# Performance work log

Measured on AMD Instinct MI355X. Metric: run time of the kernel, lower is better.

## Reference

```python
import jax, jax.numpy as jnp
import numpy as np
import math

INPUT_SZ = 1024
HIDDEN_SZ = 1024
BATCH = 64
SEQ = 512


def setup_inputs() -> dict:
    key = jax.random.key(0)
    ks = jax.random.split(key, 9)
    stdv = 1.0 / math.sqrt(HIDDEN_SZ)
    def u(k, shape):
        return jax.random.uniform(k, shape, jnp.float32, -stdv, stdv)
    W_shape = (INPUT_SZ + HIDDEN_SZ, HIDDEN_SZ)
    return {
        "x": jax.random.normal(ks[0], (BATCH, SEQ, INPUT_SZ), jnp.float32),
        "Wf": u(ks[1], W_shape), "bf": u(ks[2], (HIDDEN_SZ,)),
        "Wi": u(ks[3], W_shape), "bi": u(ks[4], (HIDDEN_SZ,)),
        "Wc": u(ks[5], W_shape), "bc": u(ks[6], (HIDDEN_SZ,)),
        "Wo": u(ks[7], W_shape), "bo": u(ks[8], (HIDDEN_SZ,)),
    }


def _lstm_cummax(x, Wf, bf, Wi, bi, Wc, bc, Wo, bo):
    B, S, _ = x.shape
    H = Wf.shape[1]
    # Concatenate the 4 gate matmuls into one GEMM (same math as 4 separate ones).
    W = jnp.concatenate([Wf, Wi, Wc, Wo], axis=1)  # (H+I, 4H)
    b = jnp.concatenate([bf, bi, bc, bo])          # (4H,)

    h0 = jnp.zeros((B, H), x.dtype)
    C0 = jnp.zeros((B, H), x.dtype)
    hmax0 = jnp.full((B, H), -jnp.inf, x.dtype)

    def step(carry, xt):
        h_in, Ct, hmax = carry
        hx = jnp.concatenate([h_in, xt], axis=1)   # (B, H+I), h first (matches torch cat((ht, xt)))
        g = hx @ W + b                             # (B, 4H)
        ft = jax.nn.sigmoid(g[:, :H])
        it = jax.nn.sigmoid(g[:, H:2 * H])
        cc = jnp.tanh(g[:, 2 * H:3 * H])
        ot = jax.nn.sigmoid(g[:, 3 * H:])
        Ct = ft * Ct + it * cc
        h = ot * jnp.tanh(Ct)                      # raw per-step hidden, stored in output seq
        hmax = jnp.maximum(hmax, h)                # running max over all steps so far
        # next-step input hidden is the running max (at t=0, max == h0 anyway)
        return (hmax, Ct, hmax), h

    (h_fin, C_fin, _), hs = jax.lax.scan(step, (h0, C0, hmax0), jnp.swapaxes(x, 0, 1))
    hidden_seq = jnp.swapaxes(hs, 0, 1)            # (B, S, H), raw per-step hiddens
    return hidden_seq, (h_fin, C_fin)


def reference(x, Wf, bf, Wi, bi, Wc, bc, Wo, bo):
    return _lstm_cummax(x, Wf, bf, Wi, bi, Wc, bc, Wo, bo)
```

## Files before the change

kernel.cpp:

```cpp
#include <hip/hip_runtime.h>
#include <hip/hip_bf16.h>
#include <math.h>
#include <stddef.h>

#define S_LEN 512
#define NBATCH 64
#define HID 1024
#define IN_SZ 1024
#define KTOT 2048
#define NB 128
#define NCOLS 32
#define JPB 8

using short8  = __attribute__((ext_vector_type(8))) short;
using floatx4 = __attribute__((ext_vector_type(4))) float;

static const size_t WPACK_OFF = 0;
static const size_t XBF_OFF   = 16777216;
static const size_t HBUF_OFF  = XBF_OFF + 67108864;
static const size_t FLAGS_OFF = HBUF_OFF + 67239936;

__device__ __forceinline__ unsigned short f2b(float f) {
  __hip_bfloat16 h = __float2bfloat16(f);
  return *reinterpret_cast<unsigned short*>(&h);
}
__device__ __forceinline__ float sigm(float z) {
  z = fminf(fmaxf(z, -30.f), 30.f);
  return 1.f / (1.f + __expf(-z));
}
__device__ __forceinline__ float tanh_(float z) {
  z = fminf(fmaxf(z, -15.f), 15.f);
  float e = __expf(2.f * z);
  return (e - 1.f) / (e + 1.f);
}

__global__ void prep_w(const float* __restrict__ Wf, const float* __restrict__ Wi,
                       const float* __restrict__ Wc, const float* __restrict__ Wo,
                       __hip_bfloat16* __restrict__ wpack) {
  __shared__ float tile[64][65];
  const int g = blockIdx.z;
  const float* W = (g == 0) ? Wf : (g == 1) ? Wi : (g == 2) ? Wc : Wo;
  const int k0 = blockIdx.x * 64, j0 = blockIdx.y * 64;
  const int tx = threadIdx.x, ty = threadIdx.y;
  for (int kk = 0; kk < 64; kk += 4)
    tile[kk + ty][tx] = W[(size_t)(k0 + kk + ty) * HID + j0 + tx];
  __syncthreads();
  for (int jj = 0; jj < 64; jj += 4) {
    int j = j0 + jj + ty;
    size_t out = ((size_t)((j >> 3) * NCOLS + g * 8 + (j & 7))) * KTOT + k0 + tx;
    wpack[out] = __float2bfloat16(tile[tx][jj + ty]);
  }
}

__global__ void prep_x(const float* __restrict__ x, unsigned short* __restrict__ xbf,
                       int* __restrict__ flags) {
  size_t i = ((size_t)blockIdx.x * blockDim.x + threadIdx.x) * 4;
  float4 v = *(const float4*)(x + i);
  ushort4 u;
  u.x = f2b(v.x); u.y = f2b(v.y); u.z = f2b(v.z); u.w = f2b(v.w);
  *(ushort4*)(xbf + i) = u;
  if (blockIdx.x == 0 && threadIdx.x < NB) flags[threadIdx.x] = 0;
}

__launch_bounds__(256, 1)
__global__ void lstm_rec(const unsigned short* __restrict__ xbf,
                         const unsigned short* __restrict__ wpack,
                         const float* __restrict__ bfv, const float* __restrict__ biv,
                         const float* __restrict__ bcv, const float* __restrict__ bov,
                         unsigned short* __restrict__ hbuf,
                         int* __restrict__ flags,
                         float* __restrict__ out) {
  __shared__ float part[4][64][36];
  const int tid  = threadIdx.x;
  const int w    = tid >> 6;
  const int lane = tid & 63;
  const int l15  = lane & 15;
  const int lq   = lane >> 4;
  const int p    = blockIdx.x;
  const int j0   = p * JPB;

  short8 Wreg[32];
  {
    const unsigned short* wp = wpack + (size_t)p * NCOLS * KTOT;
#pragma unroll
    for (int ks = 0; ks < 16; ++ks)
#pragma unroll
      for (int n = 0; n < 2; ++n) {
        int c = n * 16 + l15;
        int k = w * 512 + ks * 32 + lq * 8;
        Wreg[ks * 2 + n] = *(const short8*)(wp + (size_t)c * KTOT + k);
      }
  }
  float bias0, bias1;
  {
    int c = l15;
    bias0 = (c < 8) ? bfv[j0 + c] : biv[j0 + c - 8];
    bias1 = (c < 8) ? bcv[j0 + c] : bov[j0 + c - 8];
  }
  float Cst[4]  = {0.f, 0.f, 0.f, 0.f};
  float hmax[4] = {-__builtin_inff(), -__builtin_inff(), -__builtin_inff(), -__builtin_inff()};
  const int  jj    = l15 & 7;
  const bool act   = (l15 < 8);
  const int  bbase = w * 16 + lq * 4;
  const bool is_x  = (w >= 2);

  for (int t = 0; t < S_LEN; ++t) {
    floatx4 acc[4][2];
#pragma unroll
    for (int m = 0; m < 4; ++m) { acc[m][0] = (floatx4){0,0,0,0}; acc[m][1] = (floatx4){0,0,0,0}; }

    if (is_x) {
      const unsigned short* xa = xbf + (size_t)t * IN_SZ + (w - 2) * 512 + lq * 8;
      short8 a[16][4];
#pragma unroll
      for (int ks = 0; ks < 16; ++ks)
#pragma unroll
        for (int m = 0; m < 4; ++m)
          a[ks][m] = *(const short8*)(xa + (size_t)(m * 16 + l15) * ((size_t)S_LEN * IN_SZ) + ks * 32);
#pragma unroll
      for (int ks = 0; ks < 16; ++ks)
#pragma unroll
        for (int m = 0; m < 4; ++m) {
          acc[m][0] = __builtin_amdgcn_mfma_f32_16x16x32_bf16(a[ks][m], Wreg[ks * 2 + 0], acc[m][0], 0, 0, 0);
          acc[m][1] = __builtin_amdgcn_mfma_f32_16x16x32_bf16(a[ks][m], Wreg[ks * 2 + 1], acc[m][1], 0, 0, 0);
        }
    } else if (t > 0) {
      {
        bool ready;
        do {
          int a = __hip_atomic_load(&flags[lane],      __ATOMIC_RELAXED, __HIP_MEMORY_SCOPE_AGENT);
          int b = __hip_atomic_load(&flags[lane + 64], __ATOMIC_RELAXED, __HIP_MEMORY_SCOPE_AGENT);
          ready = __all((a >= t) && (b >= t));
        } while (!ready);
        __atomic_signal_fence(__ATOMIC_ACQUIRE);
      }
      const unsigned short* ha = hbuf + (size_t)t * (NBATCH * HID) + w * 512 + lq * 8;
      short8 a[16][4];
#pragma unroll
      for (int ks = 0; ks < 16; ++ks)
#pragma unroll
        for (int m = 0; m < 4; ++m)
          a[ks][m] = *(const short8*)(ha + (size_t)(m * 16 + l15) * HID + ks * 32);
#pragma unroll
      for (int ks = 0; ks < 16; ++ks)
#pragma unroll
        for (int m = 0; m < 4; ++m) {
          acc[m][0] = __builtin_amdgcn_mfma_f32_16x16x32_bf16(a[ks][m], Wreg[ks * 2 + 0], acc[m][0], 0, 0, 0);
          acc[m][1] = __builtin_amdgcn_mfma_f32_16x16x32_bf16(a[ks][m], Wreg[ks * 2 + 1], acc[m][1], 0, 0, 0);
        }
    }
#pragma unroll
    for (int m = 0; m < 4; ++m) {
      *(floatx4*)&part[w][lane][m * 8 + 0] = acc[m][0];
      *(floatx4*)&part[w][lane][m * 8 + 4] = acc[m][1];
    }
    __syncthreads();
    floatx4 r0 = {0, 0, 0, 0}, r1 = {0, 0, 0, 0};
#pragma unroll
    for (int sw = 0; sw < 4; ++sw) {
      r0 += *(const floatx4*)&part[sw][lane][w * 8 + 0];
      r1 += *(const floatx4*)&part[sw][lane][w * 8 + 4];
    }
#pragma unroll
    for (int r = 0; r < 4; ++r) {
      float g0  = r0[r] + bias0;
      float g1  = r1[r] + bias1;
      float g0o = __shfl_xor(g0, 8);
      float g1o = __shfl_xor(g1, 8);
      float fg = sigm(g0);
      float ig = sigm(g0o);
      float cg = tanh_(g1);
      float og = sigm(g1o);
      float C  = fg * Cst[r] + ig * cg;
      Cst[r] = C;
      float h = og * tanh_(C);
      int b = bbase + r;
      if (act)
        __builtin_nontemporal_store(
            h, &out[(size_t)b * ((size_t)S_LEN * HID) + (size_t)t * HID + j0 + jj]);
      float hm = fmaxf(hmax[r], h);
      hmax[r] = hm;
      unsigned int hb    = f2b(hm);
      unsigned int other = (unsigned int)__shfl_xor((int)hb, 1) & 0xffffu;
      if (act && ((jj & 1) == 0)) {
        unsigned int word = hb | (other << 16);
        unsigned int* dst = (unsigned int*)(hbuf + (size_t)(t + 1) * (NBATCH * HID) + (size_t)b * HID + j0 + jj);
        __hip_atomic_store(dst, word, __ATOMIC_RELAXED, __HIP_MEMORY_SCOPE_AGENT);
      }
    }
    __syncthreads();
    if (tid == 0)
      __hip_atomic_store(&flags[p], t + 1, __ATOMIC_RELAXED, __HIP_MEMORY_SCOPE_AGENT);
  }
  const size_t HSEQ = (size_t)NBATCH * S_LEN * HID;
#pragma unroll
  for (int r = 0; r < 4; ++r) {
    int b = bbase + r;
    if (act) {
      __builtin_nontemporal_store(hmax[r], &out[HSEQ + (size_t)b * HID + j0 + jj]);
      __builtin_nontemporal_store(Cst[r],  &out[HSEQ + (size_t)NBATCH * HID + (size_t)b * HID + j0 + jj]);
    }
  }
}

extern "C" void kernel_launch(void* const* d_in, const int* in_sizes, int n_in,
                              void* d_out, int out_size, void* d_ws, size_t ws_size,
                              hipStream_t stream) {
  const float* x   = (const float*)d_in[0];
  const float* Wf  = (const float*)d_in[1];
  const float* bf_ = (const float*)d_in[2];
  const float* Wi  = (const float*)d_in[3];
  const float* bi_ = (const float*)d_in[4];
  const float* Wc  = (const float*)d_in[5];
  const float* bc_ = (const float*)d_in[6];
  const float* Wo  = (const float*)d_in[7];
  const float* bo_ = (const float*)d_in[8];
  char* ws = (char*)d_ws;
  __hip_bfloat16* wpack_bf = (__hip_bfloat16*)(ws + WPACK_OFF);
  unsigned short* xbf      = (unsigned short*)(ws + XBF_OFF);
  unsigned short* hbuf     = (unsigned short*)(ws + HBUF_OFF);
  int* flags               = (int*)(ws + FLAGS_OFF);
  float* outp              = (float*)d_out;

  hipLaunchKernelGGL(prep_w, dim3(KTOT / 64, HID / 64, 4), dim3(64, 4, 1), 0, stream,
                     Wf, Wi, Wc, Wo, wpack_bf);
  hipLaunchKernelGGL(prep_x, dim3(32768), dim3(256), 0, stream, x, xbf, flags);

  lstm_rec<<<dim3(NB), dim3(256), 0, stream>>>(
      xbf, (const unsigned short*)wpack_bf, bf_, bi_, bc_, bo_, hbuf, flags, outp);
}
```

Before: 6.210 ms.

## Stage recurrent hidden-state tile into LDS via async global_load_lds with swizzle

The h-side waves now copy the previous step's bf16 hidden state straight from global memory into a 128 KB LDS buffer using async global_load_lds with an XOR swizzle, instead of loading 64 short8 registers per lane. The load is split into two halves so MFMAs on the first half overlap with the second half's transfer, gated by vmcnt waits. The partial-sum reduction buffer now aliases the same LDS, which requires an extra __syncthreads. The intent is to cut register pressure and the latency on the serial critical path. The risks are the extra barrier and the large LDS footprint.

```diff
diff --git a/kernel.cpp b/kernel.cpp
--- a/kernel.cpp
+++ b/kernel.cpp
@@ -62,6 +62,11 @@
   if (blockIdx.x == 0 && threadIdx.x < NB) flags[threadIdx.x] = 0;
 }
 
+#define GLOAD_LDS16(gp, lp)                                                              \
+  __builtin_amdgcn_global_load_lds(                                                      \
+      (const __attribute__((address_space(1))) unsigned int*)(gp),                       \
+      (__attribute__((address_space(3))) unsigned int*)(lp), 16, 0, 0)
+
 __launch_bounds__(256, 1)
 __global__ void lstm_rec(const unsigned short* __restrict__ xbf,
                          const unsigned short* __restrict__ wpack,
@@ -70,7 +75,8 @@
                          unsigned short* __restrict__ hbuf,
                          int* __restrict__ flags,
                          float* __restrict__ out) {
-  __shared__ float part[4][64][36];
+  __shared__ __align__(16) unsigned char LDSBUF[131072];
+  float* partf = (float*)LDSBUF;
   const int tid  = threadIdx.x;
   const int w    = tid >> 6;
   const int lane = tid & 63;
@@ -103,6 +109,10 @@
   const bool act   = (l15 < 8);
   const int  bbase = w * 16 + lq * 4;
   const bool is_x  = (w >= 2);
+
+  const unsigned lx   = (unsigned)lane << 4;
+  const unsigned vb   = (unsigned)l15 << 10;
+  const unsigned vcol = ((unsigned)lq << 4) ^ ((unsigned)(l15 & 7) << 4);
 
   for (int t = 0; t < S_LEN; ++t) {
     floatx4 acc[4][2];
@@ -133,33 +143,60 @@
           ready = __all((a >= t) && (b >= t));
         } while (!ready);
         __atomic_signal_fence(__ATOMIC_ACQUIRE);
-      }
-      const unsigned short* ha = hbuf + (size_t)t * (NBATCH * HID) + w * 512 + lq * 8;
-      short8 a[16][4];
-#pragma unroll
-      for (int ks = 0; ks < 16; ++ks)
-#pragma unroll
-        for (int m = 0; m < 4; ++m)
-          a[ks][m] = *(const short8*)(ha + (size_t)(m * 16 + l15) * HID + ks * 32);
-#pragma unroll
-      for (int ks = 0; ks < 16; ++ks)
-#pragma unroll
-        for (int m = 0; m < 4; ++m) {
-          acc[m][0] = __builtin_amdgcn_mfma_f32_16x16x32_bf16(a[ks][m], Wreg[ks * 2 + 0], acc[m][0], 0, 0, 0);
-          acc[m][1] = __builtin_amdgcn_mfma_f32_16x16x32_bf16(a[ks][m], Wreg[ks * 2 + 1], acc[m][1], 0, 0, 0);
-        }
-    }
-#pragma unroll
-    for (int m = 0; m < 4; ++m) {
-      *(floatx4*)&part[w][lane][m * 8 + 0] = acc[m][0];
-      *(floatx4*)&part[w][lane][m * 8 + 4] = acc[m][1];
+        asm volatile("" ::: "memory");
+      }
+      const char* gbase = (const char*)(hbuf + (size_t)t * (NBATCH * HID) + (size_t)w * 512);
+      char* lbase = (char*)LDSBUF + (w << 16);
+#pragma unroll
+      for (int i = 0; i < 32; ++i)
+        GLOAD_LDS16(gbase + (size_t)i * 2048 + (lx ^ (unsigned)((i & 7) << 4)), lbase + (i << 10));
+      __builtin_amdgcn_sched_barrier(0);
+#pragma unroll
+      for (int i = 32; i < 64; ++i)
+        GLOAD_LDS16(gbase + (size_t)i * 2048 + (lx ^ (unsigned)((i & 7) << 4)), lbase + (i << 10));
+
+      const char* hAb = (const char*)LDSBUF + (w << 16);
+      asm volatile("s_waitcnt vmcnt(32)" ::: "memory");
+      __builtin_amdgcn_sched_barrier(0);
+#pragma unroll
+      for (int ks = 0; ks < 16; ++ks) {
+        unsigned co = ((unsigned)ks << 6) ^ vcol;
+        short8 a0 = *(const short8*)(hAb + vb + co);
+        short8 a1 = *(const short8*)(hAb + 16384 + vb + co);
+        acc[0][0] = __builtin_amdgcn_mfma_f32_16x16x32_bf16(a0, Wreg[ks * 2 + 0], acc[0][0], 0, 0, 0);
+        acc[0][1] = __builtin_amdgcn_mfma_f32_16x16x32_bf16(a0, Wreg[ks * 2 + 1], acc[0][1], 0, 0, 0);
+        acc[1][0] = __builtin_amdgcn_mfma_f32_16x16x32_bf16(a1, Wreg[ks * 2 + 0], acc[1][0], 0, 0, 0);
+        acc[1][1] = __builtin_amdgcn_mfma_f32_16x16x32_bf16(a1, Wreg[ks * 2 + 1], acc[1][1], 0, 0, 0);
+      }
+      asm volatile("s_waitcnt vmcnt(0)" ::: "memory");
+      __builtin_amdgcn_sched_barrier(0);
+#pragma unroll
+      for (int ks = 0; ks < 16; ++ks) {
+        unsigned co = ((unsigned)ks << 6) ^ vcol;
+        short8 a2 = *(const short8*)(hAb + 32768 + vb + co);
+        short8 a3 = *(const short8*)(hAb + 49152 + vb + co);
+        acc[2][0] = __builtin_amdgcn_mfma_f32_16x16x32_bf16(a2, Wreg[ks * 2 + 0], acc[2][0], 0, 0, 0);
+        acc[2][1] = __builtin_amdgcn_mfma_f32_16x16x32_bf16(a2, Wreg[ks * 2 + 1], acc[2][1], 0, 0, 0);
+        acc[3][0] = __builtin_amdgcn_mfma_f32_16x16x32_bf16(a3, Wreg[ks * 2 + 0], acc[3][0], 0, 0, 0);
+        acc[3][1] = __builtin_amdgcn_mfma_f32_16x16x32_bf16(a3, Wreg[ks * 2 + 1], acc[3][1], 0, 0, 0);
+      }
+    }
+    __syncthreads();
+    {
+      float* pr = partf + (size_t)(w * 64 + lane) * 36;
+#pragma unroll
+      for (int m = 0; m < 4; ++m) {
+        *(floatx4*)(pr + m * 8 + 0) = acc[m][0];
+        *(floatx4*)(pr + m * 8 + 4) = acc[m][1];
+      }
     }
     __syncthreads();
     floatx4 r0 = {0, 0, 0, 0}, r1 = {0, 0, 0, 0};
 #pragma unroll
     for (int sw = 0; sw < 4; ++sw) {
-      r0 += *(const floatx4*)&part[sw][lane][w * 8 + 0];
-      r1 += *(const floatx4*)&part[sw][lane][w * 8 + 4];
+      const float* q = partf + (size_t)(sw * 64 + lane) * 36 + w * 8;
+      r0 += *(const floatx4*)(q);
+      r1 += *(const floatx4*)(q + 4);
     }
 #pragma unroll
     for (int r = 0; r < 4; ++r) {
```

Result: slower. 8.301 ms (+33.7%).
